# Performance work log

Measured on AMD Instinct MI355X. Metric: run time of the kernel, lower is better.

The kernel has to match this reference:

```python
import jax, jax.numpy as jnp
import numpy as np

B, N, DIM, H, DH = 2, 2048, 512, 8, 64
INNER = H * DH  # == DIM, required by the q.view trick in the original module
STEP = 4


def setup_inputs() -> dict:
    key = jax.random.key(0)
    k1, k2, k3 = jax.random.split(key, 3)
    x = jax.random.normal(k1, (B, N, DIM), jnp.float32)
    # to_qkv: Linear(dim, 4*inner_dim, bias=False); stored as [in, out] for x @ W
    W_qkv = jax.random.normal(k2, (DIM, 4 * INNER), jnp.float32) * 0.02
    # to_out: Linear(2*inner_dim, dim) with bias
    W_out = jax.random.normal(k3, (2 * INNER, DIM), jnp.float32) * 0.02
    b_out = jnp.zeros((DIM,), jnp.float32)
    return {"x": x, "W_qkv": W_qkv, "W_out": W_out, "b_out": b_out}


def reference(x, W_qkv, W_out, b_out):
    b, n, _ = x.shape
    h, dh = H, DH
    scale = dh ** -0.5

    qkvt = x @ W_qkv                       # [b, n, 4*inner]
    q, k, v, t = jnp.split(qkvt, 4, axis=-1)
    to_heads = lambda z: z.reshape(b, n, h, dh).transpose(0, 2, 1, 3)  # [b,h,n,dh]
    q, k, v, t = map(to_heads, (q, k, v, t))

    # pad q by repeating its last row yushu times (note: yushu=4 when n%4==0)
    yushu = STEP - n % STEP
    q = jnp.concatenate([q, jnp.repeat(q[:, :, -1:, :], yushu, axis=2)], axis=2)
    q0 = q.reshape(b, h, STEP, (n + yushu) // STEP, dh)[:, :, 0]  # [b,h,(n+yushu)/4,dh]
    q = jnp.tile(q0, (1, 1, STEP, 1))[:, :, :n]                   # [b,h,n,dh]

    dots = jnp.einsum('bhnd,bhmd->bhnm', q, k) * scale
    attn1 = jax.nn.softmax(dots, axis=-1)

    # fixed distance-decay attention: exp(-|i-j|/e), column-normalized
    pos = jnp.arange(1, n + 1, dtype=x.dtype)
    tg = jnp.abs(pos[None, :] - pos[:, None])                     # [n, n]
    attn2 = jnp.exp(-tg / jnp.exp(jnp.asarray(1.0, x.dtype)))
    # torch: attn2 / attn2.sum(-1) broadcasts [n] over last axis (divides column j by row-sum j)
    attn2 = attn2 / attn2.sum(-1)

    out1 = jnp.einsum('bhnm,bhmd->bhnd', attn1, v)
    out2 = jnp.einsum('nm,bhmd->bhnd', attn2, t)  # attn2 shared across b,h; no repeat needed
    out = jnp.concatenate([out1, out2], axis=-1)   # [b,h,n,2*dh]
    out = out.transpose(0, 2, 1, 3).reshape(b, n, 2 * h * dh)  # b n (h d)
    return out @ W_out + b_out  # dropout=0.0 -> identity
```

## Files before the change

### kernel.cpp

```cpp
#include <hip/hip_runtime.h>

#define NSEQ 2048
#define NB   2
#define NH   8

typedef unsigned short u16;
typedef __attribute__((ext_vector_type(8))) short s8v;
typedef __attribute__((ext_vector_type(4))) float f4v;

static __device__ __forceinline__ u16 f2bf(float f) {
  unsigned u = __float_as_uint(f);
  unsigned r = (u + 0x7fffu + ((u >> 16) & 1u)) >> 16;
  return (u16)r;
}
static __device__ __forceinline__ unsigned pk2(float a, float b) {
  return (unsigned)f2bf(a) | ((unsigned)f2bf(b) << 16);
}
static __device__ __forceinline__ float bf2f(u16 v) {
  return __uint_as_float(((unsigned)v) << 16);
}

typedef __attribute__((address_space(3))) unsigned int lds_u32;
typedef const __attribute__((address_space(1))) unsigned int glob_u32;
static __device__ __forceinline__ void load16(const void* g, void* l) {
  __builtin_amdgcn_global_load_lds((glob_u32*)g, (lds_u32*)l, 16, 0, 0);
}

__global__ __launch_bounds__(256)
void prep_kernel(const float* __restrict__ x, const float* __restrict__ Wqkv,
                 const float* __restrict__ Wout, u16* __restrict__ xb,
                 u16* __restrict__ WqkvT, u16* __restrict__ W1hi,
                 u16* __restrict__ W2hi) {
  __shared__ float tile[32][33];
  const int bid = blockIdx.x;
  if (bid < 1024) {
    long i = ((long)bid * 256 + threadIdx.x) * 8;
    float4 a = *(const float4*)&x[i];
    float4 b = *(const float4*)&x[i + 4];
    uint4 w;
    w.x = pk2(a.x, a.y); w.y = pk2(a.z, a.w);
    w.z = pk2(b.x, b.y); w.w = pk2(b.z, b.w);
    *(uint4*)&xb[i] = w;
    return;
  }
  const int tx = threadIdx.x & 31, ty = threadIdx.x >> 5;
  if (bid < 2048) {
    int b2 = bid - 1024;
    int c0 = (b2 & 63) * 32, r0 = (b2 >> 6) * 32;
#pragma unroll
    for (int s = 0; s < 32; s += 8)
      tile[ty + s][tx] = Wqkv[(long)(r0 + ty + s) * 2048 + c0 + tx];
    __syncthreads();
#pragma unroll
    for (int s = 0; s < 32; s += 8)
      WqkvT[(long)(c0 + ty + s) * 512 + r0 + tx] = f2bf(tile[tx][ty + s]);
    return;
  }
  {
    int b3 = bid - 2048;
    int part = b3 >= 256;
    if (part) b3 -= 256;
    u16* hi = part ? W2hi : W1hi;
    int c0 = (b3 & 15) * 32, r0 = (b3 >> 4) * 32;
#pragma unroll
    for (int s = 0; s < 32; s += 8) {
      int k = r0 + ty + s;
      int srcrow = ((k >> 6) * 128) + part * 64 + (k & 63);
      tile[ty + s][tx] = Wout[(long)srcrow * 512 + c0 + tx];
    }
    __syncthreads();
#pragma unroll
    for (int s = 0; s < 32; s += 8) {
      long o = (long)(c0 + ty + s) * 512 + r0 + tx;
      hi[o] = f2bf(tile[tx][ty + s]);
    }
  }
}

__global__ __launch_bounds__(256)
void gemm1_fused(const u16* __restrict__ xb, const u16* __restrict__ WqkvT,
                 u16* __restrict__ qkvtb, u16* __restrict__ qu,
                 u16* __restrict__ VtG) {
  const int bx = blockIdx.x, by = blockIdx.y;
  const bool isq = bx >= 12;
  if (isq && by >= 9) return;
  __shared__ alignas(16) u16 As[128 * 32];
  __shared__ alignas(16) u16 Bs[128 * 32];
  const int tid = threadIdx.x, lane = tid & 63, wave = tid >> 6;
  const int l15 = lane & 15, quad = lane >> 4;
  const int wr = wave >> 1, wc = wave & 1;
  const int Brow0 = isq ? (bx - 12) * 128 : 512 + bx * 128;

  f4v acc[4][4];
#pragma unroll
  for (int i = 0; i < 4; ++i)
#pragma unroll
    for (int j = 0; j < 4; ++j) acc[i][j] = (f4v){0.f, 0.f, 0.f, 0.f};

  for (int k0 = 0; k0 < 512; k0 += 32) {
    __syncthreads();
#pragma unroll
    for (int c = 0; c < 2; ++c) {
      int off = (c * 4 + wave) * 1024 + lane * 16;
      int r = off >> 6, cb = (off & 63) >> 1;
      int gar;
      if (!isq) {
        gar = by * 128 + r;
      } else {
        int rr = by * 128 + r;
        int b = rr >= 576;
        int s = rr - (b ? 576 : 0);
        if (s >= 513) s -= 513;
        gar = b * 2048 + s;
      }
      load16(&xb[(long)gar * 512 + k0 + cb], ((char*)As) + off);
      load16(&WqkvT[(long)(Brow0 + r) * 512 + k0 + cb], ((char*)Bs) + off);
    }
    __syncthreads();

    s8v bf[4];
#pragma unroll
    for (int j = 0; j < 4; ++j)
      bf[j] = *(const s8v*)&Bs[(wc * 64 + j * 16 + l15) * 32 + quad * 8];
#pragma unroll
    for (int i = 0; i < 4; ++i) {
      s8v af = *(const s8v*)&As[(wr * 64 + i * 16 + l15) * 32 + quad * 8];
#pragma unroll
      for (int j = 0; j < 4; ++j)
        acc[i][j] = __builtin_amdgcn_mfma_f32_16x16x32_bf16(af, bf[j], acc[i][j], 0, 0, 0);
    }
  }

  const bool isv = (!isq) && bx >= 4 && bx < 8;
#pragma unroll
  for (int i = 0; i < 4; ++i) {
    int row0 = by * 128 + wr * 64 + i * 16 + quad * 4;
    if (isv) {
      int b = row0 >> 11, n = row0 & 2047;
#pragma unroll
      for (int j = 0; j < 4; ++j) {
        int vcol = (bx - 4) * 128 + wc * 64 + j * 16 + l15;
        int h = vcol >> 6, d = vcol & 63;
        uint2 w;
        w.x = pk2(acc[i][j][0], acc[i][j][1]);
        w.y = pk2(acc[i][j][2], acc[i][j][3]);
        *(uint2*)&VtG[(((long)b * 8 + h) * 64 + d) * 2048 + n] = w;
      }
    } else {
#pragma unroll
      for (int rr = 0; rr < 4; ++rr) {
        int row = row0 + rr;
#pragma unroll
        for (int j = 0; j < 4; ++j) {
          int col = wc * 64 + j * 16 + l15;
          u16 v = f2bf(acc[i][j][rr]);
          if (!isq)
            qkvtb[(long)row * 2048 + 512 + bx * 128 + col] = v;
          else
            qu[(long)row * 512 + (bx - 12) * 128 + col] = v;
        }
      }
    }
  }
}

template<int BM, int BN, int TI, int TJ, bool BSPLIT, bool BIAS, bool OUTBF, bool ADDG1>
__global__ __launch_bounds__(256)
void gemm_bt_bf16(const u16* __restrict__ A, const u16* __restrict__ Bhi,
                  const u16* __restrict__ Blo, const float* __restrict__ bias,
                  const float* __restrict__ G1, void* __restrict__ Cout,
                  int M, int N, int K) {
  __shared__ alignas(16) u16 As[BM * 32];
  __shared__ alignas(16) u16 Bs[BN * 32];
  __shared__ alignas(16) u16 Bs2[BSPLIT ? BN * 32 : 8];
  const int tid = threadIdx.x, lane = tid & 63, wave = tid >> 6;
  const int l15 = lane & 15, quad = lane >> 4;
  const int wr = wave >> 1, wc = wave & 1;
  const long m0 = (long)blockIdx.y * BM, n0 = (long)blockIdx.x * BN;

  f4v acc[TI][TJ];
#pragma unroll
  for (int i = 0; i < TI; ++i)
#pragma unroll
    for (int j = 0; j < TJ; ++j) acc[i][j] = (f4v){0.f, 0.f, 0.f, 0.f};

  for (int k0 = 0; k0 < K; k0 += 32) {
    __syncthreads();
#pragma unroll
    for (int c = 0; c < BM / 64; ++c) {
      int off = (c * 4 + wave) * 1024 + lane * 16;
      int r = off >> 6, cb = (off & 63) >> 1;
      load16(&A[(m0 + r) * K + k0 + cb], ((char*)As) + off);
    }
#pragma unroll
    for (int c = 0; c < BN / 64; ++c) {
      int off = (c * 4 + wave) * 1024 + lane * 16;
      int r = off >> 6, cb = (off & 63) >> 1;
      load16(&Bhi[(n0 + r) * K + k0 + cb], ((char*)Bs) + off);
      if constexpr (BSPLIT)
        load16(&Blo[(n0 + r) * K + k0 + cb], ((char*)Bs2) + off);
    }
    __syncthreads();

    s8v bf[TJ], bf2[BSPLIT ? TJ : 1];
#pragma unroll
    for (int j = 0; j < TJ; ++j) {
      bf[j] = *(const s8v*)&Bs[(wc * (TJ * 16) + j * 16 + l15) * 32 + quad * 8];
      if constexpr (BSPLIT)
        bf2[j] = *(const s8v*)&Bs2[(wc * (TJ * 16) + j * 16 + l15) * 32 + quad * 8];
    }
#pragma unroll
    for (int i = 0; i < TI; ++i) {
      s8v af = *(const s8v*)&As[(wr * (TI * 16) + i * 16 + l15) * 32 + quad * 8];
#pragma unroll
      for (int j = 0; j < TJ; ++j) {
        acc[i][j] = __builtin_amdgcn_mfma_f32_16x16x32_bf16(af, bf[j], acc[i][j], 0, 0, 0);
        if constexpr (BSPLIT)
          acc[i][j] = __builtin_amdgcn_mfma_f32_16x16x32_bf16(af, bf2[j], acc[i][j], 0, 0, 0);
      }
    }
  }

#pragma unroll
  for (int i = 0; i < TI; ++i)
#pragma unroll
    for (int rr = 0; rr < 4; ++rr) {
      long row = m0 + wr * (TI * 16) + i * 16 + quad * 4 + rr;
      long g1row = 0;
      if constexpr (ADDG1)
        g1row = (long)((int)(row >> 11) * 576 + ((int)(row & 2047) % 513)) * 512;
#pragma unroll
      for (int j = 0; j < TJ; ++j) {
        long col = n0 + wc * (TJ * 16) + j * 16 + l15;
        float v = acc[i][j][rr];
        if constexpr (BIAS) v += bias[col];
        if constexpr (ADDG1) v += G1[g1row + col];
        if constexpr (OUTBF)
          ((u16*)Cout)[row * N + col] = f2bf(v);
        else
          ((float*)Cout)[row * N + col] = v;
      }
    }
}

__global__ __launch_bounds__(256)
void attn_kernel(const u16* __restrict__ qkvt, const u16* __restrict__ qu,
                 const u16* __restrict__ VtG, float* __restrict__ Opart,
                 float* __restrict__ rspart) {
  __shared__ alignas(16) u16 Qs[64 * 64];
  __shared__ alignas(16) u16 Ks[64 * 64];
  __shared__ alignas(16) u16 Vt[64 * 64];
  __shared__ alignas(16) u16 Ps[4][16][72];

  const int tid  = threadIdx.x;
  const int lane = tid & 63, wave = tid >> 6;
  const int l15  = lane & 15, quad = lane >> 4;
  const int qtile = blockIdx.x;
  const int bh = blockIdx.y;
  const int split = blockIdx.z;
  const int b = bh >> 3, h = bh & 7;
  const long rowbase = (long)b * NSEQ;
  const long vtbase = ((long)b * 8 + h) * 64 * 2048;

  int srow[2], scs[2];
#pragma unroll
  for (int p = 0; p < 2; ++p) {
    int idx = p * 256 + tid;
    srow[p] = idx >> 3;
    scs[p] = (idx & 7) ^ (srow[p] & 7);
  }

#pragma unroll
  for (int p = 0; p < 2; ++p) {
    int v = qtile * 64 + srow[p];
    int eff = v >= 513 ? v - 513 : v;
    load16(&qu[((long)(b * 576 + eff)) * 512 + h * 64 + scs[p] * 8],
           (char*)Qs + (p * 256 + wave * 64) * 16);
  }
  __syncthreads();

  s8v qf[2];
  {
    const int mrow = wave * 16 + l15;
    const int c0 = quad ^ (mrow & 7);
    qf[0] = *(const s8v*)&Qs[mrow * 64 + c0 * 8];
    qf[1] = *(const s8v*)&Qs[mrow * 64 + (c0 ^ 4) * 8];
  }

  f4v oacc[4];
#pragma unroll
  for (int i = 0; i < 4; ++i) oacc[i] = (f4v){0.f, 0.f, 0.f, 0.f};
  float rs[4] = {0.f, 0.f, 0.f, 0.f};

  for (int kt = 0; kt < 8; ++kt) {
    __syncthreads();
    const int kb = split * 512 + kt * 64;
#pragma unroll
    for (int p = 0; p < 2; ++p) {
      load16(&qkvt[(rowbase + kb + srow[p]) * 2048 + 512 + h * 64 + scs[p] * 8],
             (char*)Ks + (p * 256 + wave * 64) * 16);
      load16(&VtG[vtbase + (long)srow[p] * 2048 + kb + scs[p] * 8],
             (char*)Vt + (p * 256 + wave * 64) * 16);
    }
    __syncthreads();

#pragma unroll
    for (int nt = 0; nt < 4; ++nt) {
      f4v s = {0.f, 0.f, 0.f, 0.f};
      const int kr = nt * 16 + l15;
      const int kc0 = quad ^ (kr & 7);
      s8v kf0 = *(const s8v*)&Ks[kr * 64 + kc0 * 8];
      s8v kf1 = *(const s8v*)&Ks[kr * 64 + (kc0 ^ 4) * 8];
      s = __builtin_amdgcn_mfma_f32_16x16x32_bf16(qf[0], kf0, s, 0, 0, 0);
      s = __builtin_amdgcn_mfma_f32_16x16x32_bf16(qf[1], kf1, s, 0, 0, 0);
#pragma unroll
      for (int rr = 0; rr < 4; ++rr) {
        float p = __expf(s[rr] * 0.125f);
        rs[rr] += p;
        Ps[wave][quad * 4 + rr][nt * 16 + l15] = f2bf(p);
      }
    }
    asm volatile("" ::: "memory");

    s8v pf0 = *(const s8v*)&Ps[wave][l15][quad * 8];
    s8v pf1 = *(const s8v*)&Ps[wave][l15][32 + quad * 8];
#pragma unroll
    for (int nt = 0; nt < 4; ++nt) {
      const int vr = nt * 16 + l15;
      const int vc0 = quad ^ (vr & 7);
      s8v vf0 = *(const s8v*)&Vt[vr * 64 + vc0 * 8];
      s8v vf1 = *(const s8v*)&Vt[vr * 64 + (vc0 ^ 4) * 8];
      oacc[nt] = __builtin_amdgcn_mfma_f32_16x16x32_bf16(pf0, vf0, oacc[nt], 0, 0, 0);
      oacc[nt] = __builtin_amdgcn_mfma_f32_16x16x32_bf16(pf1, vf1, oacc[nt], 0, 0, 0);
    }
  }

  const long sb = ((long)split * 16 + bh) * 576;
#pragma unroll
  for (int rr = 0; rr < 4; ++rr) {
    float t = rs[rr];
    t += __shfl_xor(t, 1);
    t += __shfl_xor(t, 2);
    t += __shfl_xor(t, 4);
    t += __shfl_xor(t, 8);
    int row = qtile * 64 + wave * 16 + quad * 4 + rr;
    if (l15 == 0) rspart[sb + row] = t;
#pragma unroll
    for (int nt = 0; nt < 4; ++nt)
      Opart[(sb + row) * 64 + nt * 16 + l15] = oacc[nt][rr];
  }
}

__global__ __launch_bounds__(256)
void attn_combine(const float* __restrict__ Opart, const float* __restrict__ rspart,
                  u16* __restrict__ O1u) {
  int idx = blockIdx.x * 256 + threadIdx.x;
  int d4 = idx & 15, rowbh = idx >> 4;
  int bh = rowbh / 576, row = rowbh - bh * 576;
  int b = bh >> 3, h = bh & 7;
  float4 o = {0.f, 0.f, 0.f, 0.f};
  float rsum = 0.f;
#pragma unroll
  for (int s = 0; s < 4; ++s) {
    long base = ((long)s * 16 + bh) * 576 + row;
    float4 v = *(const float4*)&Opart[base * 64 + d4 * 4];
    o.x += v.x; o.y += v.y; o.z += v.z; o.w += v.w;
    rsum += rspart[base];
  }
  float inv = 1.0f / rsum;
  unsigned w0 = pk2(o.x * inv, o.y * inv);
  unsigned w1 = pk2(o.z * inv, o.w * inv);
  uint2 w = {w0, w1};
  *(uint2*)&O1u[((long)(b * 576 + row)) * 512 + h * 64 + d4 * 4] = w;
}

__global__ __launch_bounds__(256)
void out2_kernel(const u16* __restrict__ qkvt, u16* __restrict__ O2) {
  __shared__ u16 Ts[256 * 64];
  __shared__ float Is[256];
  const int tid = threadIdx.x;
  const int rg = blockIdx.x;
  const int bh = blockIdx.y;
  const int b = bh >> 3, h = bh & 7;
  const int g0 = rg * 64 - 96;
#pragma unroll
  for (int c = 0; c < 8; ++c) {
    int chunk = c * 256 + tid;
    int row = chunk >> 3, cc = chunk & 7;
    int gr = g0 + row;
    uint4 w = {0u, 0u, 0u, 0u};
    if (gr >= 0 && gr < NSEQ)
      w = *(const uint4*)&qkvt[((long)(b * NSEQ + gr)) * 2048 + 1536 + h * 64 + cc * 8];
    *(uint4*)&Ts[row * 64 + cc * 8] = w;
  }
  {
    const float ie = 0.36787944117144233f;
    const float rr = 0.69220062755534635f;
    const float inv1mr = 1.0f / (1.0f - rr);
    int gr = g0 + tid;
    float val = 0.f;
    if (gr >= 0 && gr < NSEQ) {
      float rj = __expf(-ie * (float)gr);
      float rn = __expf(-ie * (float)(NSEQ - 1 - gr));
      float s = 1.0f + (rr - rr * rj) * inv1mr + (rr - rr * rn) * inv1mr;
      val = 1.0f / s;
    }
    Is[tid] = val;
  }
  __syncthreads();

  const int d = tid & 63, sub = tid >> 6;
  const float r = 0.69220062755534635f;
  const int lo = 96 + sub * 16;
  float F = 0.f;
  float Fv[16];
#pragma unroll 8
  for (int j = lo - 96; j < lo; ++j)
    F = F * r + Is[j] * bf2f(Ts[j * 64 + d]);
#pragma unroll
  for (int k = 0; k < 16; ++k) {
    int j = lo + k;
    F = F * r + Is[j] * bf2f(Ts[j * 64 + d]);
    Fv[k] = F;
  }
  float G = 0.f;
#pragma unroll 8
  for (int j = lo + 15 + 96; j > lo + 15; --j)
    G = G * r + Is[j] * bf2f(Ts[j * 64 + d]);
#pragma unroll
  for (int k = 15; k >= 0; --k) {
    int j = lo + k;
    float u = Is[j] * bf2f(Ts[j * 64 + d]);
    G = G * r + u;
    O2[((long)(b * NSEQ + g0 + j)) * 512 + h * 64 + d] = f2bf(Fv[k] + G - u);
  }
}

extern "C" void kernel_launch(void* const* d_in, const int* in_sizes, int n_in,
                              void* d_out, int out_size, void* d_ws, size_t ws_size,
                              hipStream_t stream) {
  (void)in_sizes; (void)n_in; (void)out_size; (void)ws_size;
  const float* x    = (const float*)d_in[0];
  const float* Wqkv = (const float*)d_in[1];
  const float* Wout = (const float*)d_in[2];
  const float* bout = (const float*)d_in[3];
  float* out = (float*)d_out;

  u16*   qkvtb = (u16*)d_ws;
  u16*   qu    = qkvtb + (size_t)4096 * 2048;
  u16*   VtG   = qu    + (size_t)1152 * 512;
  u16*   O2    = VtG   + (size_t)2 * 8 * 64 * 2048;
  u16*   O1u   = O2    + (size_t)4096 * 512;
  u16*   xb    = O1u   + (size_t)1152 * 512;
  u16*   WqkvT = xb    + (size_t)4096 * 512;
  u16*   W1hi  = WqkvT + (size_t)2048 * 512;
  u16*   W2hi  = W1hi  + (size_t)512 * 512;
  float* Opart = (float*)(W2hi + (size_t)512 * 512);
  float* rsp   = Opart + (size_t)4 * 16 * 576 * 64;
  float* G1    = Opart;

  prep_kernel<<<dim3(2560), 256, 0, stream>>>(x, Wqkv, Wout, xb, WqkvT, W1hi, W2hi);
  gemm1_fused<<<dim3(16, 32), 256, 0, stream>>>(xb, WqkvT, qkvtb, qu, VtG);
  attn_kernel<<<dim3(9, 16, 4), 256, 0, stream>>>(qkvtb, qu, VtG, Opart, rsp);
  attn_combine<<<dim3(576), 256, 0, stream>>>(Opart, rsp, O1u);
  out2_kernel<<<dim3(32, 16), 256, 0, stream>>>(qkvtb, O2);
  gemm_bt_bf16<128, 64, 4, 2, false, false, false, false>
      <<<dim3(8, 9), 256, 0, stream>>>(O1u, W1hi, nullptr, nullptr, nullptr,
                                       G1, 1152, 512, 512);
  gemm_bt_bf16<128, 64, 4, 2, false, true, false, true>
      <<<dim3(8, 32), 256, 0, stream>>>(O2, W2hi, nullptr, bout, G1,
                                        out, 4096, 512, 512);
}
```

Baseline: 139.0 us.

## Use 32x32x16 MFMA in GEMMs and merge combine with out2 kernel

Switches the QKV projection and both output GEMMs from 16x16x32 to 32x32x16 bf16 MFMA tiles, which cuts LDS fragment reads per MFMA and uses larger accumulator tiles. The generic templated GEMM becomes a specialised fixed-size kernel with the bias load hoisted and the G1 row modulo computed once per tile. The attention-combine and out2 kernels are merged into one launch, dispatched by block index, to save a launch and let the two independent jobs overlap. The epilogue store patterns change, and the stores for non-V outputs stay scattered 2-byte writes.

```diff
diff --git a/kernel.cpp b/kernel.cpp
--- a/kernel.cpp
+++ b/kernel.cpp
@@ -7,6 +7,7 @@
 typedef unsigned short u16;
 typedef __attribute__((ext_vector_type(8))) short s8v;
 typedef __attribute__((ext_vector_type(4))) float f4v;
+typedef __attribute__((ext_vector_type(16))) float f16v;
 
 static __device__ __forceinline__ u16 f2bf(float f) {
   unsigned u = __float_as_uint(f);
@@ -87,15 +88,17 @@
   __shared__ alignas(16) u16 As[128 * 32];
   __shared__ alignas(16) u16 Bs[128 * 32];
   const int tid = threadIdx.x, lane = tid & 63, wave = tid >> 6;
-  const int l15 = lane & 15, quad = lane >> 4;
+  const int l31 = lane & 31, half = lane >> 5;
   const int wr = wave >> 1, wc = wave & 1;
   const int Brow0 = isq ? (bx - 12) * 128 : 512 + bx * 128;
 
-  f4v acc[4][4];
-#pragma unroll
-  for (int i = 0; i < 4; ++i)
-#pragma unroll
-    for (int j = 0; j < 4; ++j) acc[i][j] = (f4v){0.f, 0.f, 0.f, 0.f};
+  f16v acc[2][2];
+#pragma unroll
+  for (int i = 0; i < 2; ++i)
+#pragma unroll
+    for (int j = 0; j < 2; ++j)
+#pragma unroll
+      for (int r = 0; r < 16; ++r) acc[i][j][r] = 0.f;
 
   for (int k0 = 0; k0 < 512; k0 += 32) {
     __syncthreads();
@@ -118,42 +121,50 @@
     }
     __syncthreads();
 
-    s8v bf[4];
-#pragma unroll
-    for (int j = 0; j < 4; ++j)
-      bf[j] = *(const s8v*)&Bs[(wc * 64 + j * 16 + l15) * 32 + quad * 8];
-#pragma unroll
-    for (int i = 0; i < 4; ++i) {
-      s8v af = *(const s8v*)&As[(wr * 64 + i * 16 + l15) * 32 + quad * 8];
-#pragma unroll
-      for (int j = 0; j < 4; ++j)
-        acc[i][j] = __builtin_amdgcn_mfma_f32_16x16x32_bf16(af, bf[j], acc[i][j], 0, 0, 0);
+    s8v bf[2][2];
+#pragma unroll
+    for (int tj = 0; tj < 2; ++tj)
+#pragma unroll
+      for (int kh = 0; kh < 2; ++kh)
+        bf[tj][kh] = *(const s8v*)&Bs[(wc * 64 + tj * 32 + l31) * 32 + kh * 16 + half * 8];
+#pragma unroll
+    for (int ti = 0; ti < 2; ++ti) {
+      s8v af[2];
+#pragma unroll
+      for (int kh = 0; kh < 2; ++kh)
+        af[kh] = *(const s8v*)&As[(wr * 64 + ti * 32 + l31) * 32 + kh * 16 + half * 8];
+#pragma unroll
+      for (int tj = 0; tj < 2; ++tj)
+#pragma unroll
+        for (int kh = 0; kh < 2; ++kh)
+          acc[ti][tj] = __builtin_amdgcn_mfma_f32_32x32x16_bf16(af[kh], bf[tj][kh],
+                                                                acc[ti][tj], 0, 0, 0);
     }
   }
 
   const bool isv = (!isq) && bx >= 4 && bx < 8;
 #pragma unroll
-  for (int i = 0; i < 4; ++i) {
-    int row0 = by * 128 + wr * 64 + i * 16 + quad * 4;
-    if (isv) {
-      int b = row0 >> 11, n = row0 & 2047;
-#pragma unroll
-      for (int j = 0; j < 4; ++j) {
-        int vcol = (bx - 4) * 128 + wc * 64 + j * 16 + l15;
+  for (int ti = 0; ti < 2; ++ti)
+#pragma unroll
+    for (int tj = 0; tj < 2; ++tj) {
+      if (isv) {
+        int vcol = (bx - 4) * 128 + wc * 64 + tj * 32 + l31;
         int h = vcol >> 6, d = vcol & 63;
-        uint2 w;
-        w.x = pk2(acc[i][j][0], acc[i][j][1]);
-        w.y = pk2(acc[i][j][2], acc[i][j][3]);
-        *(uint2*)&VtG[(((long)b * 8 + h) * 64 + d) * 2048 + n] = w;
-      }
-    } else {
-#pragma unroll
-      for (int rr = 0; rr < 4; ++rr) {
-        int row = row0 + rr;
-#pragma unroll
-        for (int j = 0; j < 4; ++j) {
-          int col = wc * 64 + j * 16 + l15;
-          u16 v = f2bf(acc[i][j][rr]);
+#pragma unroll
+        for (int g = 0; g < 4; ++g) {
+          int nrow = by * 128 + wr * 64 + ti * 32 + g * 8 + half * 4;
+          int b = nrow >> 11, n = nrow & 2047;
+          uint2 w;
+          w.x = pk2(acc[ti][tj][4 * g + 0], acc[ti][tj][4 * g + 1]);
+          w.y = pk2(acc[ti][tj][4 * g + 2], acc[ti][tj][4 * g + 3]);
+          *(uint2*)&VtG[(((long)b * 8 + h) * 64 + d) * 2048 + n] = w;
+        }
+      } else {
+        int col = wc * 64 + tj * 32 + l31;
+#pragma unroll
+        for (int reg = 0; reg < 16; ++reg) {
+          int row = by * 128 + wr * 64 + ti * 32 + (reg & 3) + 8 * (reg >> 2) + half * 4;
+          u16 v = f2bf(acc[ti][tj][reg]);
           if (!isq)
             qkvtb[(long)row * 2048 + 512 + bx * 128 + col] = v;
           else
@@ -161,86 +172,80 @@
         }
       }
     }
-  }
-}
-
-template<int BM, int BN, int TI, int TJ, bool BSPLIT, bool BIAS, bool OUTBF, bool ADDG1>
+}
+
+template<bool BIAS, bool ADDG1>
 __global__ __launch_bounds__(256)
-void gemm_bt_bf16(const u16* __restrict__ A, const u16* __restrict__ Bhi,
-                  const u16* __restrict__ Blo, const float* __restrict__ bias,
-                  const float* __restrict__ G1, void* __restrict__ Cout,
-                  int M, int N, int K) {
-  __shared__ alignas(16) u16 As[BM * 32];
-  __shared__ alignas(16) u16 Bs[BN * 32];
-  __shared__ alignas(16) u16 Bs2[BSPLIT ? BN * 32 : 8];
+void gemm2_bt(const u16* __restrict__ A, const u16* __restrict__ B,
+              const float* __restrict__ bias, const float* __restrict__ G1,
+              float* __restrict__ C) {
+  __shared__ alignas(16) u16 As[128 * 32];
+  __shared__ alignas(16) u16 Bs[64 * 32];
   const int tid = threadIdx.x, lane = tid & 63, wave = tid >> 6;
-  const int l15 = lane & 15, quad = lane >> 4;
+  const int l31 = lane & 31, half = lane >> 5;
   const int wr = wave >> 1, wc = wave & 1;
-  const long m0 = (long)blockIdx.y * BM, n0 = (long)blockIdx.x * BN;
-
-  f4v acc[TI][TJ];
-#pragma unroll
-  for (int i = 0; i < TI; ++i)
-#pragma unroll
-    for (int j = 0; j < TJ; ++j) acc[i][j] = (f4v){0.f, 0.f, 0.f, 0.f};
-
-  for (int k0 = 0; k0 < K; k0 += 32) {
-    __syncthreads();
-#pragma unroll
-    for (int c = 0; c < BM / 64; ++c) {
+  const long m0 = (long)blockIdx.y * 128, n0 = (long)blockIdx.x * 64;
+
+  f16v acc[2];
+#pragma unroll
+  for (int i = 0; i < 2; ++i)
+#pragma unroll
+    for (int r = 0; r < 16; ++r) acc[i][r] = 0.f;
+
+  for (int k0 = 0; k0 < 512; k0 += 32) {
+    __syncthreads();
+#pragma unroll
+    for (int c = 0; c < 2; ++c) {
       int off = (c * 4 + wave) * 1024 + lane * 16;
       int r = off >> 6, cb = (off & 63) >> 1;
-      load16(&A[(m0 + r) * K + k0 + cb], ((char*)As) + off);
-    }
-#pragma unroll
-    for (int c = 0; c < BN / 64; ++c) {
-      int off = (c * 4 + wave) * 1024 + lane * 16;
+      load16(&A[(m0 + r) * 512 + k0 + cb], ((char*)As) + off);
+    }
+    {
+      int off = wave * 1024 + lane * 16;
       int r = off >> 6, cb = (off & 63) >> 1;
-      load16(&Bhi[(n0 + r) * K + k0 + cb], ((char*)Bs) + off);
-      if constexpr (BSPLIT)
-        load16(&Blo[(n0 + r) * K + k0 + cb], ((char*)Bs2) + off);
-    }
-    __syncthreads();
-
-    s8v bf[TJ], bf2[BSPLIT ? TJ : 1];
-#pragma unroll
-    for (int j = 0; j < TJ; ++j) {
-      bf[j] = *(const s8v*)&Bs[(wc * (TJ * 16) + j * 16 + l15) * 32 + quad * 8];
-      if constexpr (BSPLIT)
-        bf2[j] = *(const s8v*)&Bs2[(wc * (TJ * 16) + j * 16 + l15) * 32 + quad * 8];
-    }
-#pragma unroll
-    for (int i = 0; i < TI; ++i) {
-      s8v af = *(const s8v*)&As[(wr * (TI * 16) + i * 16 + l15) * 32 + quad * 8];
-#pragma unroll
-      for (int j = 0; j < TJ; ++j) {
-        acc[i][j] = __builtin_amdgcn_mfma_f32_16x16x32_bf16(af, bf[j], acc[i][j], 0, 0, 0);
-        if constexpr (BSPLIT)
-          acc[i][j] = __builtin_amdgcn_mfma_f32_16x16x32_bf16(af, bf2[j], acc[i][j], 0, 0, 0);
+      load16(&B[(n0 + r) * 512 + k0 + cb], ((char*)Bs) + off);
+    }
+    __syncthreads();
+
+    s8v bf[2];
+#pragma unroll
+    for (int kh = 0; kh < 2; ++kh)
+      bf[kh] = *(const s8v*)&Bs[(wc * 32 + l31) * 32 + kh * 16 + half * 8];
+#pragma unroll
+    for (int ti = 0; ti < 2; ++ti) {
+      s8v af[2];
+#pragma unroll
+      for (int kh = 0; kh < 2; ++kh)
+        af[kh] = *(const s8v*)&As[(wr * 64 + ti * 32 + l31) * 32 + kh * 16 + half * 8];
+#pragma unroll
+      for (int kh = 0; kh < 2; ++kh)
+        acc[ti] = __builtin_amdgcn_mfma_f32_32x32x16_bf16(af[kh], bf[kh], acc[ti], 0, 0, 0);
+    }
+  }
+
+  const long col = n0 + wc * 32 + l31;
+  float bv = 0.f;
+  if constexpr (BIAS) bv = bias[col];
+#pragma unroll
+  for (int ti = 0; ti < 2; ++ti) {
+    long rbase = m0 + wr * 64 + ti * 32;
+    int sbase = 0;
+    if constexpr (ADDG1)
+      sbase = (int)((rbase >> 11) * 576) ;
+    int smod = (int)(rbase & 2047) % 513;
+#pragma unroll
+    for (int reg = 0; reg < 16; ++reg) {
+      int rmap = (reg & 3) + 8 * (reg >> 2) + half * 4;
+      long row = rbase + rmap;
+      float v = acc[ti][reg] + bv;
+      if constexpr (ADDG1) {
+        int sr = smod + rmap;
+        if (sr >= 513) sr -= 513;
+        v += G1[(long)(sbase + sr) * 512 + col];
       }
-    }
-  }
-
-#pragma unroll
-  for (int i = 0; i < TI; ++i)
-#pragma unroll
-    for (int rr = 0; rr < 4; ++rr) {
-      long row = m0 + wr * (TI * 16) + i * 16 + quad * 4 + rr;
-      long g1row = 0;
-      if constexpr (ADDG1)
-        g1row = (long)((int)(row >> 11) * 576 + ((int)(row & 2047) % 513)) * 512;
-#pragma unroll
-      for (int j = 0; j < TJ; ++j) {
-        long col = n0 + wc * (TJ * 16) + j * 16 + l15;
-        float v = acc[i][j][rr];
-        if constexpr (BIAS) v += bias[col];
-        if constexpr (ADDG1) v += G1[g1row + col];
-        if constexpr (OUTBF)
-          ((u16*)Cout)[row * N + col] = f2bf(v);
-        else
-          ((float*)Cout)[row * N + col] = v;
-      }
-    }
+      C[row * 512 + col] = v;
+    }
+  }
 }
 
 __global__ __launch_bounds__(256)
@@ -352,35 +357,34 @@
 }
 
 __global__ __launch_bounds__(256)
-void attn_combine(const float* __restrict__ Opart, const float* __restrict__ rspart,
-                  u16* __restrict__ O1u) {
-  int idx = blockIdx.x * 256 + threadIdx.x;
-  int d4 = idx & 15, rowbh = idx >> 4;
-  int bh = rowbh / 576, row = rowbh - bh * 576;
-  int b = bh >> 3, h = bh & 7;
-  float4 o = {0.f, 0.f, 0.f, 0.f};
-  float rsum = 0.f;
-#pragma unroll
-  for (int s = 0; s < 4; ++s) {
-    long base = ((long)s * 16 + bh) * 576 + row;
-    float4 v = *(const float4*)&Opart[base * 64 + d4 * 4];
-    o.x += v.x; o.y += v.y; o.z += v.z; o.w += v.w;
-    rsum += rspart[base];
-  }
-  float inv = 1.0f / rsum;
-  unsigned w0 = pk2(o.x * inv, o.y * inv);
-  unsigned w1 = pk2(o.z * inv, o.w * inv);
-  uint2 w = {w0, w1};
-  *(uint2*)&O1u[((long)(b * 576 + row)) * 512 + h * 64 + d4 * 4] = w;
-}
-
-__global__ __launch_bounds__(256)
-void out2_kernel(const u16* __restrict__ qkvt, u16* __restrict__ O2) {
+void post_kernel(const u16* __restrict__ qkvt, const float* __restrict__ Opart,
+                 const float* __restrict__ rspart, u16* __restrict__ O1u,
+                 u16* __restrict__ O2) {
   __shared__ u16 Ts[256 * 64];
   __shared__ float Is[256];
   const int tid = threadIdx.x;
-  const int rg = blockIdx.x;
-  const int bh = blockIdx.y;
+  const int bid = blockIdx.x;
+  if (bid >= 512) {
+    int idx = (bid - 512) * 256 + tid;
+    int d4 = idx & 15, rowbh = idx >> 4;
+    int bh = rowbh / 576, row = rowbh - bh * 576;
+    int b = bh >> 3, h = bh & 7;
+    float4 o = {0.f, 0.f, 0.f, 0.f};
+    float rsum = 0.f;
+#pragma unroll
+    for (int s = 0; s < 4; ++s) {
+      long base = ((long)s * 16 + bh) * 576 + row;
+      float4 v = *(const float4*)&Opart[base * 64 + d4 * 4];
+      o.x += v.x; o.y += v.y; o.z += v.z; o.w += v.w;
+      rsum += rspart[base];
+    }
+    float inv = 1.0f / rsum;
+    uint2 w = {pk2(o.x * inv, o.y * inv), pk2(o.z * inv, o.w * inv)};
+    *(uint2*)&O1u[((long)(b * 576 + row)) * 512 + h * 64 + d4 * 4] = w;
+    return;
+  }
+  const int rg = bid & 31;
+  const int bh = bid >> 5;
   const int b = bh >> 3, h = bh & 7;
   const int g0 = rg * 64 - 96;
 #pragma unroll
@@ -462,12 +466,7 @@
   prep_kernel<<<dim3(2560), 256, 0, stream>>>(x, Wqkv, Wout, xb, WqkvT, W1hi, W2hi);
   gemm1_fused<<<dim3(16, 32), 256, 0, stream>>>(xb, WqkvT, qkvtb, qu, VtG);
   attn_kernel<<<dim3(9, 16, 4), 256, 0, stream>>>(qkvtb, qu, VtG, Opart, rsp);
-  attn_combine<<<dim3(576), 256, 0, stream>>>(Opart, rsp, O1u);
-  out2_kernel<<<dim3(32, 16), 256, 0, stream>>>(qkvtb, O2);
-  gemm_bt_bf16<128, 64, 4, 2, false, false, false, false>
-      <<<dim3(8, 9), 256, 0, stream>>>(O1u, W1hi, nullptr, nullptr, nullptr,
-                                       G1, 1152, 512, 512);
-  gemm_bt_bf16<128, 64, 4, 2, false, true, false, true>
-      <<<dim3(8, 32), 256, 0, stream>>>(O2, W2hi, nullptr, bout, G1,
-                                        out, 4096, 512, 512);
-}
+  post_kernel<<<dim3(1088), 256, 0, stream>>>(qkvtb, Opart, rsp, O1u, O2);
+  gemm2_bt<false, false><<<dim3(8, 9), 256, 0, stream>>>(O1u, W1hi, nullptr, nullptr, G1);
+  gemm2_bt<true, true><<<dim3(8, 32), 256, 0, stream>>>(O2, W2hi, bout, G1, out);
+}
```

Result: slower. 147.6 us (+6.2%).
